# Performance work log

Hardware: AMD Instinct MI355X
Metric: run time of the kernel (lower is better)

## Reference

```python
import jax, jax.numpy as jnp
import numpy as np

EPS = 1e-12  # F.normalize eps


def setup_inputs() -> dict:
    key = jax.random.key(0)
    k1, k2 = jax.random.split(key)
    bs, d = 8192, 128
    data = jax.random.normal(k1, (bs, d), dtype=jnp.float32)
    label = jax.random.randint(k2, (bs, 1), 0, 2, dtype=jnp.int64)
    scale = jnp.asarray(np.log(1.0 / 0.07), dtype=jnp.float32)  # learned temperature param
    return {"data": data, "scale": scale, "label": label}


def reference(data, scale, label):
    bs = data.shape[0]
    # L2-normalize rows (F.normalize semantics with eps clamp)
    norm = jnp.maximum(jnp.linalg.norm(data, axis=-1, keepdims=True), EPS)
    x = data / norm
    logits = (x @ x.T) * jnp.exp(scale)  # [bs, bs]
    # Vectorized equivalent of the python double loop: binary same-class matrix
    sim = (label == label.T).astype(logits.dtype)  # [bs, bs]
    q = jax.nn.softmax(sim / jnp.sum(sim, axis=-1, keepdims=True), axis=-1)
    p = jax.nn.log_softmax(logits, axis=-1)
    log_q = jnp.log(q)  # q > 0 always (softmax output)
    # F.kl_div(p, q, 'batchmean') = sum(q * (log q - p)) / bs
    loss1 = jnp.sum(q * (log_q - p)) / bs
    # F.kl_div(q.log(), p.exp(), 'batchmean') = sum(exp(p) * (p - log q)) / bs
    loss2 = jnp.sum(jnp.exp(p) * (p - log_q)) / bs
    return (loss1 + loss2) * 0.5
```

## Files before the change

### kernel.cpp

```cpp
#include <hip/hip_runtime.h>
#include <stdint.h>

#define BS 8192
#define DD 128
#define SPLIT 8

typedef __attribute__((ext_vector_type(8))) short short8;
typedef __attribute__((ext_vector_type(4))) float float4v;

__device__ __forceinline__ float bf2f(short s) {
  union { unsigned u; float f; } c;
  c.u = ((unsigned)(unsigned short)s) << 16;
  return c.f;
}
__device__ __forceinline__ short f2bf(float f) {
  union { float f; unsigned u; } c; c.f = f;
  unsigned u = c.u + 0x7FFFu + ((c.u >> 16) & 1u);
  return (short)(u >> 16);
}

__global__ __launch_bounds__(256) void k_norm(const float* __restrict__ data,
                                              const int* __restrict__ label,
                                              unsigned int* __restrict__ xnb32,
                                              float* __restrict__ xnf,
                                              float* __restrict__ gh,
                                              int* __restrict__ cnt) {
  __shared__ float sh[256];
  __shared__ int shc[2];
  int tid = threadIdx.x, wave = tid >> 6, lane = tid & 63;
  if (tid < 2) shc[tid] = 0;
  sh[tid] = 0.f;
  __syncthreads();
  float a00 = 0.f, a01 = 0.f, a10 = 0.f, a11 = 0.f;
  int c0 = 0, c1 = 0;
  int rbase = blockIdx.x * 32 + wave * 8;
  for (int r = 0; r < 8; ++r) {
    int row = rbase + r;
    float2 v = *(const float2*)&data[row * DD + lane * 2];
    float ss = v.x * v.x + v.y * v.y;
    for (int off = 32; off; off >>= 1) ss += __shfl_xor(ss, off);
    float rn = 1.f / fmaxf(sqrtf(ss), 1e-12f);
    float x0 = v.x * rn, x1 = v.y * rn;
    *(float2*)&xnf[row * DD + lane * 2] = make_float2(x0, x1);
    unsigned int pk = (unsigned int)(unsigned short)f2bf(x0) |
                      ((unsigned int)(unsigned short)f2bf(x1) << 16);
    xnb32[row * 64 + lane] = pk;
    int lab = label[row];
    if (lab == 0) { a00 += x0; a01 += x1; c0++; }
    else          { a10 += x0; a11 += x1; c1++; }
  }
  atomicAdd(&sh[2 * lane], a00);
  atomicAdd(&sh[2 * lane + 1], a01);
  atomicAdd(&sh[128 + 2 * lane], a10);
  atomicAdd(&sh[128 + 2 * lane + 1], a11);
  if (lane == 0) { atomicAdd(&shc[0], c0); atomicAdd(&shc[1], c1); }
  __syncthreads();
  atomicAdd(&gh[tid], sh[tid]);
  if (tid < 2) atomicAdd(&cnt[tid], shc[tid]);
}

__global__ __launch_bounds__(256) void k_main(const unsigned short* __restrict__ xnb,
                                              const int* __restrict__ label,
                                              const float* __restrict__ scale,
                                              float* __restrict__ Zr,
                                              float* __restrict__ Ur,
                                              float* __restrict__ Vr) {
  __shared__ short tile[64 * DD];
  int tid = threadIdx.x, wave = tid >> 6, lane = tid & 63;
  int quad = lane >> 4, col = lane & 15;
  int rb = blockIdx.x / SPLIT, sl = blockIdx.x % SPLIT;
  float se = __expf(scale[0]);

  int arow = rb * 64 + wave * 16 + col;
  const short* ap = (const short*)xnb + (size_t)arow * DD;
  short8 afrag[4];
#pragma unroll
  for (int t = 0; t < 4; ++t) {
    short8 a = *(const short8*)(ap + t * 32 + quad * 8);
#pragma unroll
    for (int i = 0; i < 8; ++i) a[i] = f2bf(bf2f(a[i]) * se);
    afrag[t] = a;
  }
  int labI[4];
#pragma unroll
  for (int r = 0; r < 4; ++r) labI[r] = label[rb * 64 + wave * 16 + quad * 4 + r];

  float Z[4] = {0, 0, 0, 0}, U[4] = {0, 0, 0, 0}, V0[4] = {0, 0, 0, 0};

  const char* srcbase = (const char*)xnb;
  int rowloc = tid >> 4;
  int swz = (tid & 15) ^ rowloc;
  for (int j0 = sl * (BS / SPLIT); j0 < (sl + 1) * (BS / SPLIT); j0 += 64) {
    __syncthreads();
    char* dst = ((char*)tile) + tid * 16;
#pragma unroll
    for (int p = 0; p < 4; ++p) {
      const char* src = srcbase + (size_t)(j0 + p * 16 + rowloc) * 256 + swz * 16;
      __builtin_amdgcn_global_load_lds(
          (const __attribute__((address_space(1))) void*)(uintptr_t)src,
          (__attribute__((address_space(3))) void*)(uintptr_t)(dst + p * 4096), 16, 0, 0);
    }
    __syncthreads();
#pragma unroll
    for (int jo = 0; jo < 4; ++jo) {
      int jc = j0 + jo * 16 + col;
      float m0 = (label[jc] == 0) ? 1.f : 0.f;
      float4v c = {0.f, 0.f, 0.f, 0.f};
      const short* bp = tile + (jo * 16 + col) * DD;
#pragma unroll
      for (int t = 0; t < 4; ++t) {
        short8 b = *(const short8*)(bp + (((t * 4 + quad) ^ col)) * 8);
        c = __builtin_amdgcn_mfma_f32_16x16x32_bf16(afrag[t], b, c, 0, 0, 0);
      }
#pragma unroll
      for (int r = 0; r < 4; ++r) {
        float l = c[r];
        float e = __expf(l);
        Z[r] += e;
        U[r] += e * l;
        V0[r] += m0 * e;
      }
    }
  }
#pragma unroll
  for (int r = 0; r < 4; ++r) {
#pragma unroll
    for (int off = 1; off < 16; off <<= 1) {
      Z[r] += __shfl_xor(Z[r], off);
      U[r] += __shfl_xor(U[r], off);
      V0[r] += __shfl_xor(V0[r], off);
    }
  }
  if (col == 0) {
#pragma unroll
    for (int r = 0; r < 4; ++r) {
      int row = rb * 64 + wave * 16 + quad * 4 + r;
      float v = (labI[r] == 0) ? V0[r] : (Z[r] - V0[r]);
      atomicAdd(&Zr[row], Z[r]);
      atomicAdd(&Ur[row], U[r]);
      atomicAdd(&Vr[row], v);
    }
  }
}

__global__ __launch_bounds__(256) void k_final(const float* __restrict__ xnf,
                                               const int* __restrict__ label,
                                               const float* __restrict__ scale,
                                               const float* __restrict__ gh,
                                               const int* __restrict__ cnt,
                                               const float* __restrict__ Zr,
                                               const float* __restrict__ Ur,
                                               const float* __restrict__ Vr,
                                               float* __restrict__ out) {
  __shared__ float bsum[4];
  int tid = threadIdx.x, wave = tid >> 6, lane = tid & 63;
  float se = __expf(scale[0]);
  float h0a = gh[2 * lane], h0b = gh[2 * lane + 1];
  float h1a = gh[128 + 2 * lane], h1b = gh[128 + 2 * lane + 1];
  float ga = h0a + h1a, gb = h0b + h1b;
  float c0 = (float)cnt[0], c1 = (float)cnt[1];
  float local = 0.f;
  int rbase = blockIdx.x * 32 + wave * 8;
  for (int r = 0; r < 8; ++r) {
    int row = rbase + r;
    float2 x = *(const float2*)&xnf[row * DD + lane * 2];
    int lab = label[row];
    float sg = x.x * ga + x.y * gb;
    float sh_ = (lab == 0) ? (x.x * h0a + x.y * h0b) : (x.x * h1a + x.y * h1b);
    for (int off = 32; off; off >>= 1) {
      sg += __shfl_xor(sg, off);
      sh_ += __shfl_xor(sh_, off);
    }
    if (lane == 0) {
      float cc = (lab == 0) ? c0 : c1;
      float a = __expf(1.f / cc);
      float Zq = cc * a + ((float)BS - cc);
      float S = se * sg, T = se * sh_;
      float Z = Zr[row], U = Ur[row], V = Vr[row];
      local += a / Zq - (S + (a - 1.f) * T) / Zq + U / Z - V / (cc * Z);
    }
  }
  if (lane == 0) bsum[wave] = local;
  __syncthreads();
  if (tid == 0) {
    float s = bsum[0] + bsum[1] + bsum[2] + bsum[3];
    atomicAdd(out, s * (0.5f / (float)BS));
  }
}

extern "C" void kernel_launch(void* const* d_in, const int* in_sizes, int n_in,
                              void* d_out, int out_size, void* d_ws, size_t ws_size,
                              hipStream_t stream) {
  const float* data = (const float*)d_in[0];
  const float* scale = (const float*)d_in[1];
  const int* label = (const int*)d_in[2];
  char* ws = (char*)d_ws;
  unsigned short* xnb = (unsigned short*)ws;
  unsigned int* xnb32 = (unsigned int*)ws;
  float* xnf = (float*)(ws + 2097152);
  float* Zr = (float*)(ws + 6291456);
  float* Ur = (float*)(ws + 6324224);
  float* Vr = (float*)(ws + 6356992);
  float* gh = (float*)(ws + 6389760);
  int* cnt = (int*)(ws + 6390784);

  hipMemsetAsync(ws + 6291456, 0, 99336, stream);
  hipMemsetAsync(d_out, 0, sizeof(float), stream);

  k_norm<<<256, 256, 0, stream>>>(data, label, xnb32, xnf, gh, cnt);
  k_main<<<128 * SPLIT, 256, 0, stream>>>(xnb, label, scale, Zr, Ur, Vr);
  k_final<<<256, 256, 0, stream>>>(xnf, label, scale, gh, cnt, Zr, Ur, Vr, (float*)d_out);
}
```

Measured before the change: 122.1 us.

## Process two A row-tiles per block to reuse B tiles and fold zeroing into k_norm

Each k_main block now holds A fragments for 128 rows (two 16-row subtiles per wave) and issues two MFMAs per loaded B fragment. This halves LDS/global B traffic per useful FLOP. SPLIT doubles so the grid stays at 1024 blocks. The Zr/Ur/Vr and output zeroing moves from a memset into k_norm, leaving a single small memset and so less launch overhead. The cost is more registers for the doubled accumulators and fragments, which may lower occupancy.

```diff
diff --git a/kernel.cpp b/kernel.cpp
--- a/kernel.cpp
+++ b/kernel.cpp
@@ -3,7 +3,7 @@
 
 #define BS 8192
 #define DD 128
-#define SPLIT 8
+#define SPLIT 16
 
 typedef __attribute__((ext_vector_type(8))) short short8;
 typedef __attribute__((ext_vector_type(4))) float float4v;
@@ -24,12 +24,21 @@
                                               unsigned int* __restrict__ xnb32,
                                               float* __restrict__ xnf,
                                               float* __restrict__ gh,
-                                              int* __restrict__ cnt) {
+                                              int* __restrict__ cnt,
+                                              float* __restrict__ Zr,
+                                              float* __restrict__ Ur,
+                                              float* __restrict__ Vr,
+                                              float* __restrict__ out) {
   __shared__ float sh[256];
   __shared__ int shc[2];
   int tid = threadIdx.x, wave = tid >> 6, lane = tid & 63;
   if (tid < 2) shc[tid] = 0;
   sh[tid] = 0.f;
+  if (tid < 32) {
+    int row = blockIdx.x * 32 + tid;
+    Zr[row] = 0.f; Ur[row] = 0.f; Vr[row] = 0.f;
+  }
+  if (blockIdx.x == 0 && tid == 0) out[0] = 0.f;
   __syncthreads();
   float a00 = 0.f, a01 = 0.f, a10 = 0.f, a11 = 0.f;
   int c0 = 0, c1 = 0;
@@ -71,21 +80,25 @@
   int rb = blockIdx.x / SPLIT, sl = blockIdx.x % SPLIT;
   float se = __expf(scale[0]);
 
-  int arow = rb * 64 + wave * 16 + col;
-  const short* ap = (const short*)xnb + (size_t)arow * DD;
-  short8 afrag[4];
-#pragma unroll
-  for (int t = 0; t < 4; ++t) {
-    short8 a = *(const short8*)(ap + t * 32 + quad * 8);
-#pragma unroll
-    for (int i = 0; i < 8; ++i) a[i] = f2bf(bf2f(a[i]) * se);
-    afrag[t] = a;
-  }
-  int labI[4];
-#pragma unroll
-  for (int r = 0; r < 4; ++r) labI[r] = label[rb * 64 + wave * 16 + quad * 4 + r];
-
-  float Z[4] = {0, 0, 0, 0}, U[4] = {0, 0, 0, 0}, V0[4] = {0, 0, 0, 0};
+  short8 afrag[2][4];
+  int labI[2][4];
+#pragma unroll
+  for (int s = 0; s < 2; ++s) {
+    int arow = rb * 128 + s * 64 + wave * 16 + col;
+    const short* ap = (const short*)xnb + (size_t)arow * DD;
+#pragma unroll
+    for (int t = 0; t < 4; ++t) {
+      short8 a = *(const short8*)(ap + t * 32 + quad * 8);
+#pragma unroll
+      for (int i = 0; i < 8; ++i) a[i] = f2bf(bf2f(a[i]) * se);
+      afrag[s][t] = a;
+    }
+#pragma unroll
+    for (int r = 0; r < 4; ++r)
+      labI[s][r] = label[rb * 128 + s * 64 + wave * 16 + quad * 4 + r];
+  }
+
+  float Z[2][4] = {}, U[2][4] = {}, V0[2][4] = {};
 
   const char* srcbase = (const char*)xnb;
   int rowloc = tid >> 4;
@@ -105,41 +118,44 @@
     for (int jo = 0; jo < 4; ++jo) {
       int jc = j0 + jo * 16 + col;
       float m0 = (label[jc] == 0) ? 1.f : 0.f;
-      float4v c = {0.f, 0.f, 0.f, 0.f};
+      float4v c0 = {0.f, 0.f, 0.f, 0.f}, c1 = {0.f, 0.f, 0.f, 0.f};
       const short* bp = tile + (jo * 16 + col) * DD;
 #pragma unroll
       for (int t = 0; t < 4; ++t) {
-        short8 b = *(const short8*)(bp + (((t * 4 + quad) ^ col)) * 8);
-        c = __builtin_amdgcn_mfma_f32_16x16x32_bf16(afrag[t], b, c, 0, 0, 0);
+        short8 b = *(const short8*)(bp + ((t * 4 + quad) ^ col) * 8);
+        c0 = __builtin_amdgcn_mfma_f32_16x16x32_bf16(afrag[0][t], b, c0, 0, 0, 0);
+        c1 = __builtin_amdgcn_mfma_f32_16x16x32_bf16(afrag[1][t], b, c1, 0, 0, 0);
       }
 #pragma unroll
       for (int r = 0; r < 4; ++r) {
-        float l = c[r];
-        float e = __expf(l);
-        Z[r] += e;
-        U[r] += e * l;
-        V0[r] += m0 * e;
-      }
-    }
-  }
-#pragma unroll
-  for (int r = 0; r < 4; ++r) {
-#pragma unroll
-    for (int off = 1; off < 16; off <<= 1) {
-      Z[r] += __shfl_xor(Z[r], off);
-      U[r] += __shfl_xor(U[r], off);
-      V0[r] += __shfl_xor(V0[r], off);
-    }
-  }
+        float l0 = c0[r], e0 = __expf(l0);
+        Z[0][r] += e0; U[0][r] += e0 * l0; V0[0][r] += m0 * e0;
+        float l1 = c1[r], e1 = __expf(l1);
+        Z[1][r] += e1; U[1][r] += e1 * l1; V0[1][r] += m0 * e1;
+      }
+    }
+  }
+#pragma unroll
+  for (int s = 0; s < 2; ++s)
+#pragma unroll
+    for (int r = 0; r < 4; ++r)
+#pragma unroll
+      for (int off = 1; off < 16; off <<= 1) {
+        Z[s][r] += __shfl_xor(Z[s][r], off);
+        U[s][r] += __shfl_xor(U[s][r], off);
+        V0[s][r] += __shfl_xor(V0[s][r], off);
+      }
   if (col == 0) {
 #pragma unroll
-    for (int r = 0; r < 4; ++r) {
-      int row = rb * 64 + wave * 16 + quad * 4 + r;
-      float v = (labI[r] == 0) ? V0[r] : (Z[r] - V0[r]);
-      atomicAdd(&Zr[row], Z[r]);
-      atomicAdd(&Ur[row], U[r]);
-      atomicAdd(&Vr[row], v);
-    }
+    for (int s = 0; s < 2; ++s)
+#pragma unroll
+      for (int r = 0; r < 4; ++r) {
+        int row = rb * 128 + s * 64 + wave * 16 + quad * 4 + r;
+        float v = (labI[s][r] == 0) ? V0[s][r] : (Z[s][r] - V0[s][r]);
+        atomicAdd(&Zr[row], Z[s][r]);
+        atomicAdd(&Ur[row], U[s][r]);
+        atomicAdd(&Vr[row], v);
+      }
   }
 }
 
@@ -204,10 +220,10 @@
   float* gh = (float*)(ws + 6389760);
   int* cnt = (int*)(ws + 6390784);
 
-  hipMemsetAsync(ws + 6291456, 0, 99336, stream);
-  hipMemsetAsync(d_out, 0, sizeof(float), stream);
-
-  k_norm<<<256, 256, 0, stream>>>(data, label, xnb32, xnf, gh, cnt);
-  k_main<<<128 * SPLIT, 256, 0, stream>>>(xnb, label, scale, Zr, Ur, Vr);
+  hipMemsetAsync(ws + 6389760, 0, 1032, stream);
+
+  k_norm<<<256, 256, 0, stream>>>(data, label, xnb32, xnf, gh, cnt, Zr, Ur, Vr,
+                                  (float*)d_out);
+  k_main<<<64 * SPLIT, 256, 0, stream>>>(xnb, label, scale, Zr, Ur, Vr);
   k_final<<<256, 256, 0, stream>>>(xnf, label, scale, gh, cnt, Zr, Ur, Vr, (float*)d_out);
 }
```

New measurement: 125.0 us. +2.4%, slower.
